# Kernel tuning notes

Measured on AMD Instinct MI355X. Metric: run time of the kernel, lower is better.

## Reference

```python
import jax, jax.numpy as jnp
import numpy as np

T, BATCH, DMODEL, H = 2048, 16, 512, 512


def setup_inputs() -> dict:
    key = jax.random.key(0)
    ks = jax.random.split(key, 8)
    x = jax.random.normal(ks[0], (T, BATCH, DMODEL), jnp.float32)
    # initial carry: (lambda=1, h=0) so the concat trick leaves state untouched
    h0_re = jnp.zeros((1, BATCH, H), jnp.float32)
    h0_im = jnp.zeros((1, BATCH, H), jnp.float32)
    # LRU parameterization (Orvieto et al. 2023): |lambda| in [0.9, 0.99]
    u1 = jax.random.uniform(ks[1], (H,), jnp.float32)
    nu_log = jnp.log(-0.5 * jnp.log(u1 * (0.99 ** 2 - 0.9 ** 2) + 0.9 ** 2))
    theta_log = jnp.log(jax.random.uniform(ks[2], (H,), jnp.float32) * (np.pi / 10) + 1e-4)
    B_re = jax.random.normal(ks[3], (H, DMODEL), jnp.float32) / np.sqrt(2 * DMODEL)
    B_im = jax.random.normal(ks[4], (H, DMODEL), jnp.float32) / np.sqrt(2 * DMODEL)
    C_re = jax.random.normal(ks[5], (DMODEL, H), jnp.float32) / np.sqrt(H)
    C_im = jax.random.normal(ks[6], (DMODEL, H), jnp.float32) / np.sqrt(H)
    D_vec = jax.random.normal(ks[7], (DMODEL,), jnp.float32)
    return dict(x=x, h0_re=h0_re, h0_im=h0_im, nu_log=nu_log, theta_log=theta_log,
                B_re=B_re, B_im=B_im, C_re=C_re, C_im=C_im, D_vec=D_vec)


def _binop(qi, qj):
    # associative combine for h_t = a_t * h_{t-1} + b_t
    a_i, b_i = qi
    a_j, b_j = qj
    return (a_j * a_i, a_j * b_i + b_j)


def reference(x, h0_re, h0_im, nu_log, theta_log, B_re, B_im, C_re, C_im, D_vec):
    # diagonal complex recurrence eigenvalues, |Lambda| = exp(-exp(nu_log)) < 1
    Lam = jnp.exp(-jnp.exp(nu_log) + 1j * jnp.exp(theta_log))        # [H] complex64
    gamma = jnp.sqrt(1.0 - jnp.exp(-2.0 * jnp.exp(nu_log)))           # [H]
    Bmat = (B_re + 1j * B_im) * gamma[:, None]                         # [H, D]
    # map_to_h: Bu elements and broadcast Lambda elements
    Bu = jnp.einsum('tbd,hd->tbh', x.astype(jnp.complex64), Bmat)      # [T, B, H]
    Lam_el = jnp.broadcast_to(Lam, Bu.shape)                            # [T, B, H]
    # concat previous state (lambda=1, b=h0) as first scan element
    h0 = (h0_re + 1j * h0_im).astype(jnp.complex64)                    # [1, B, H]
    a = jnp.concatenate([jnp.ones_like(h0), Lam_el], axis=0)          # [T+1, B, H]
    b = jnp.concatenate([h0, Bu], axis=0)                              # [T+1, B, H]
    _, h_all = jax.lax.associative_scan(_binop, (a, b), axis=0)
    h = h_all[1:]                                                       # [T, B, H]
    # map_from_h: y = Re(C h) + D * x (elementwise skip)
    Cmat = C_re + 1j * C_im                                             # [D, H]
    y = jnp.einsum('tbh,dh->tbd', h, Cmat).real + D_vec * x            # [T, B, D]
    final_state = h[-1:]                                                # [1, B, H]
    return (final_state, y)
```

## Files before the change

### kernel.cpp

```cpp
#include <hip/hip_runtime.h>
#include <stdint.h>

typedef short shortx8 __attribute__((ext_vector_type(8)));
typedef float floatx4 __attribute__((ext_vector_type(4)));

#define T_LEN 2048
#define BATCH 16
#define DMODEL 512
#define HDIM 512
#define M_ROWS (T_LEN * BATCH)
#define NCHUNK 32
#define LCHUNK 64
#define NCHAIN (BATCH * HDIM)
#define Y_ELEMS (M_ROWS * DMODEL)

__device__ __forceinline__ unsigned short f2bf(float f) {
    union { float f; unsigned u; } v; v.f = f;
    unsigned r = (v.u + 0x7FFFu + ((v.u >> 16) & 1u)) >> 16;
    return (unsigned short)r;
}
__device__ __forceinline__ float bf2f(unsigned short u) {
    union { unsigned u; float f; } v; v.u = ((unsigned)u) << 16;
    return v.f;
}

__global__ void prep_kernel(const float* __restrict__ nu_log, const float* __restrict__ th_log,
                            float* lam_re, float* lam_im, float* l64_re, float* l64_im, float* gam) {
    int h = blockIdx.x * blockDim.x + threadIdx.x;
    if (h >= HDIM) return;
    double nu  = exp((double)nu_log[h]);
    double th  = exp((double)th_log[h]);
    double mag = exp(-nu);
    double lre = mag * cos(th), lim = mag * sin(th);
    double g   = sqrt(1.0 - exp(-2.0 * nu));
    double zr = lre, zi = lim;
    for (int i = 0; i < 6; ++i) { double nr = zr*zr - zi*zi; zi = 2.0*zr*zi; zr = nr; }
    lam_re[h] = (float)lre; lam_im[h] = (float)lim;
    l64_re[h] = (float)zr;  l64_im[h] = (float)zi;
    gam[h] = (float)g;
}

__global__ void conv_BC_kernel(const float* __restrict__ B_re, const float* __restrict__ B_im,
                               const float* __restrict__ gam,
                               const float* __restrict__ C_re, const float* __restrict__ C_im,
                               unsigned short* __restrict__ Bs, unsigned short* __restrict__ C2) {
    int idx = blockIdx.x * blockDim.x + threadIdx.x;
    if (idx < 524288) {
        int n = idx >> 9;
        int d = idx & 511;
        int h = n & 511;
        float v = (n < HDIM ? B_re[h * DMODEL + d] : B_im[h * DMODEL + d]) * gam[h];
        Bs[idx] = f2bf(v);
    } else {
        int i2 = idx - 524288;
        int d = i2 >> 10;
        int k = i2 & 1023;
        float v = (k < HDIM) ? C_re[d * HDIM + k] : -C_im[d * HDIM + (k - HDIM)];
        C2[i2] = f2bf(v);
    }
}

__global__ void cast_x_kernel(const float4* __restrict__ x4, unsigned short* __restrict__ xb, int n4) {
    int i = blockIdx.x * blockDim.x + threadIdx.x;
    if (i >= n4) return;
    float4 v = x4[i];
    ushort4 u;
    u.x = f2bf(v.x); u.y = f2bf(v.y); u.z = f2bf(v.z); u.w = f2bf(v.w);
    *(ushort4*)(xb + (size_t)i * 4) = u;
}

template <int MODE>
__global__ __launch_bounds__(256, 4) void gemm_nt(const unsigned short* __restrict__ A,
                                                  const unsigned short* __restrict__ Bmat,
                                                  const int K, const int N, const int lgNB,
                                                  unsigned short* __restrict__ OutB,
                                                  float* __restrict__ OutF,
                                                  const float* __restrict__ Dv,
                                                  const unsigned short* __restrict__ Xb) {
    __shared__ unsigned short As[128 * 64];
    __shared__ unsigned short Bs[128 * 64];
    const int L = blockIdx.x;
    const int xcd = L & 7;
    const int slot = L >> 3;
    const int bn = slot & ((1 << lgNB) - 1);
    const int bm = xcd * 32 + (slot >> lgNB);
    const int tid = threadIdx.x;
    const int wv = tid >> 6, lane = tid & 63;
    const int wr = wv >> 1, wc = wv & 1;
    const int lrow = lane & 15, qq = lane >> 4;
    floatx4 acc[4][4] = {};

    const size_t rowA = (size_t)bm * 128, rowB = (size_t)bn * 128;
    for (int k0 = 0; k0 < K; k0 += 64) {
        #pragma unroll
        for (int j = 0; j < 4; ++j) {
            int ch  = j * 256 + wv * 64 + lane;
            int r   = ch >> 3;
            int c16 = ch & 7;
            int g16 = c16 ^ (r & 7);
            const unsigned short* ga = A    + (rowA + r) * (size_t)K + (k0 + g16 * 8);
            const unsigned short* gb = Bmat + (rowB + r) * (size_t)K + (k0 + g16 * 8);
            unsigned short* la = As + (size_t)(j * 256 + wv * 64) * 8;
            unsigned short* lb = Bs + (size_t)(j * 256 + wv * 64) * 8;
            __builtin_amdgcn_global_load_lds((const __attribute__((address_space(1))) void*)ga,
                                             (__attribute__((address_space(3))) void*)la, 16, 0, 0);
            __builtin_amdgcn_global_load_lds((const __attribute__((address_space(1))) void*)gb,
                                             (__attribute__((address_space(3))) void*)lb, 16, 0, 0);
        }
        __syncthreads();
        #pragma unroll
        for (int s = 0; s < 2; ++s) {
            shortx8 af[4], bf[4];
            #pragma unroll
            for (int mi = 0; mi < 4; ++mi) {
                int row = wr * 64 + mi * 16 + lrow;
                int c16 = (s * 4 + qq) ^ (row & 7);
                af[mi] = *(const shortx8*)&As[row * 64 + c16 * 8];
            }
            #pragma unroll
            for (int ni = 0; ni < 4; ++ni) {
                int row = wc * 64 + ni * 16 + lrow;
                int c16 = (s * 4 + qq) ^ (row & 7);
                bf[ni] = *(const shortx8*)&Bs[row * 64 + c16 * 8];
            }
            #pragma unroll
            for (int mi = 0; mi < 4; ++mi)
                #pragma unroll
                for (int ni = 0; ni < 4; ++ni)
                    acc[mi][ni] = __builtin_amdgcn_mfma_f32_16x16x32_bf16(af[mi], bf[ni], acc[mi][ni], 0, 0, 0);
        }
        __syncthreads();
    }

    #pragma unroll
    for (int mi = 0; mi < 4; ++mi) {
        int mbase = bm * 128 + wr * 64 + mi * 16 + qq * 4;
        #pragma unroll
        for (int ni = 0; ni < 4; ++ni) {
            int n = bn * 128 + wc * 64 + ni * 16 + lrow;
            if (MODE == 0) {
                #pragma unroll
                for (int r = 0; r < 4; ++r)
                    OutB[(size_t)(mbase + r) * N + n] = f2bf(acc[mi][ni][r]);
            } else {
                float dv = Dv[n];
                #pragma unroll
                for (int r = 0; r < 4; ++r) {
                    size_t idx = (size_t)(mbase + r) * N + n;
                    OutF[idx] = acc[mi][ni][r] + dv * bf2f(Xb[idx]);
                }
            }
        }
    }
}

__global__ void scan_partial(const unsigned short* __restrict__ Bu,
                             const float* __restrict__ lam_re, const float* __restrict__ lam_im,
                             float* __restrict__ car_re, float* __restrict__ car_im) {
    int gid = blockIdx.x * blockDim.x + threadIdx.x;
    int chunk = gid >> 12;
    int idx = gid & 4095;
    int b = idx >> 8, hp = idx & 255;
    int h = hp * 2;
    float lr0 = lam_re[h], li0 = lam_im[h];
    float lr1 = lam_re[h + 1], li1 = lam_im[h + 1];
    float v0r = 0.f, v0i = 0.f, v1r = 0.f, v1i = 0.f;
    const unsigned short* p = Bu + (size_t)chunk * LCHUNK * BATCH * 1024 + (size_t)b * 1024 + h;
    for (int j = 0; j < LCHUNK; ++j) {
        unsigned rr = *(const unsigned*)p;
        unsigned ii = *(const unsigned*)(p + 512);
        float b0r = bf2f((unsigned short)rr), b1r = bf2f((unsigned short)(rr >> 16));
        float b0i = bf2f((unsigned short)ii), b1i = bf2f((unsigned short)(ii >> 16));
        float n0r = lr0 * v0r - li0 * v0i + b0r;
        float n0i = lr0 * v0i + li0 * v0r + b0i;
        float n1r = lr1 * v1r - li1 * v1i + b1r;
        float n1i = lr1 * v1i + li1 * v1r + b1i;
        v0r = n0r; v0i = n0i; v1r = n1r; v1i = n1i;
        p += BATCH * 1024;
    }
    int c = b * 512 + h;
    *(float2*)&car_re[chunk * NCHAIN + c] = make_float2(v0r, v1r);
    *(float2*)&car_im[chunk * NCHAIN + c] = make_float2(v0i, v1i);
}

__global__ void scan_apply(unsigned short* __restrict__ Bu,
                           const float* __restrict__ lam_re, const float* __restrict__ lam_im,
                           const float* __restrict__ l64_re, const float* __restrict__ l64_im,
                           const float* __restrict__ h0_re, const float* __restrict__ h0_im,
                           const float* __restrict__ car_re, const float* __restrict__ car_im,
                           float* __restrict__ out_final, int interleave) {
    int gid = blockIdx.x * blockDim.x + threadIdx.x;
    int chunk = gid >> 12;
    int idx = gid & 4095;
    int b = idx >> 8, hp = idx & 255;
    int h = hp * 2;
    int c = b * 512 + h;
    float L0r = l64_re[h], L0i = l64_im[h];
    float L1r = l64_re[h + 1], L1i = l64_im[h + 1];
    float v0r = h0_re[c], v0i = h0_im[c];
    float v1r = h0_re[c + 1], v1i = h0_im[c + 1];
    for (int k = 0; k < chunk; ++k) {
        float2 crr = *(const float2*)&car_re[k * NCHAIN + c];
        float2 cii = *(const float2*)&car_im[k * NCHAIN + c];
        float n0r = L0r * v0r - L0i * v0i + crr.x;
        float n0i = L0r * v0i + L0i * v0r + cii.x;
        float n1r = L1r * v1r - L1i * v1i + crr.y;
        float n1i = L1r * v1i + L1i * v1r + cii.y;
        v0r = n0r; v0i = n0i; v1r = n1r; v1i = n1i;
    }
    float lr0 = lam_re[h], li0 = lam_im[h];
    float lr1 = lam_re[h + 1], li1 = lam_im[h + 1];
    unsigned short* p = Bu + (size_t)chunk * LCHUNK * BATCH * 1024 + (size_t)b * 1024 + h;
    for (int j = 0; j < LCHUNK; ++j) {
        unsigned rr = *(const unsigned*)p;
        unsigned ii = *(const unsigned*)(p + 512);
        float b0r = bf2f((unsigned short)rr), b1r = bf2f((unsigned short)(rr >> 16));
        float b0i = bf2f((unsigned short)ii), b1i = bf2f((unsigned short)(ii >> 16));
        float n0r = lr0 * v0r - li0 * v0i + b0r;
        float n0i = lr0 * v0i + li0 * v0r + b0i;
        float n1r = lr1 * v1r - li1 * v1i + b1r;
        float n1i = lr1 * v1i + li1 * v1r + b1i;
        v0r = n0r; v0i = n0i; v1r = n1r; v1i = n1i;
        *(unsigned*)p         = (unsigned)f2bf(v0r) | ((unsigned)f2bf(v1r) << 16);
        *(unsigned*)(p + 512) = (unsigned)f2bf(v0i) | ((unsigned)f2bf(v1i) << 16);
        p += BATCH * 1024;
    }
    if (chunk == NCHUNK - 1) {
        if (interleave) {
            out_final[2 * c]     = v0r;
            out_final[2 * c + 1] = v0i;
            out_final[2 * c + 2] = v1r;
            out_final[2 * c + 3] = v1i;
        } else {
            out_final[c]     = v0r;
            out_final[c + 1] = v1r;
        }
    }
}

extern "C" void kernel_launch(void* const* d_in, const int* in_sizes, int n_in,
                              void* d_out, int out_size, void* d_ws, size_t ws_size,
                              hipStream_t stream) {
    const float* x        = (const float*)d_in[0];
    const float* h0_re    = (const float*)d_in[1];
    const float* h0_im    = (const float*)d_in[2];
    const float* nu_log   = (const float*)d_in[3];
    const float* theta_lg = (const float*)d_in[4];
    const float* B_re     = (const float*)d_in[5];
    const float* B_im     = (const float*)d_in[6];
    const float* C_re     = (const float*)d_in[7];
    const float* C_im     = (const float*)d_in[8];
    const float* D_vec    = (const float*)d_in[9];

    char* ws = (char*)d_ws;
    unsigned short* BuH  = (unsigned short*)(ws + 0);
    unsigned short* xb   = (unsigned short*)(ws + 67108864);
    unsigned short* Bs   = (unsigned short*)(ws + 100663296);
    unsigned short* C2   = (unsigned short*)(ws + 101711872);
    float* car_re        = (float*)(ws + 102760448);
    float* car_im        = (float*)(ws + 103809024);
    float* lam_re        = (float*)(ws + 104857600);
    float* lam_im        = (float*)(ws + 104859648);
    float* l64_re        = (float*)(ws + 104861696);
    float* l64_im        = (float*)(ws + 104863744);
    float* gam           = (float*)(ws + 104865792);

    int fs_elems = out_size - Y_ELEMS;
    int interleave = (fs_elems == 8192) ? 0 : 1;
    if (fs_elems != 8192) fs_elems = 16384;
    float* out_final = (float*)d_out;
    float* y_out     = (float*)d_out + fs_elems;

    prep_kernel<<<2, 256, 0, stream>>>(nu_log, theta_lg, lam_re, lam_im, l64_re, l64_im, gam);
    conv_BC_kernel<<<(1048576) / 256, 256, 0, stream>>>(B_re, B_im, gam, C_re, C_im, Bs, C2);
    cast_x_kernel<<<(Y_ELEMS / 4) / 256, 256, 0, stream>>>((const float4*)x, xb, Y_ELEMS / 4);
    gemm_nt<0><<<2048, 256, 0, stream>>>(xb, Bs, DMODEL, 1024, 3, BuH, nullptr, nullptr, nullptr);
    scan_partial<<<(NCHUNK * NCHAIN / 2) / 256, 256, 0, stream>>>(BuH, lam_re, lam_im, car_re, car_im);
    scan_apply<<<(NCHUNK * NCHAIN / 2) / 256, 256, 0, stream>>>(BuH, lam_re, lam_im, l64_re, l64_im,
                                                                h0_re, h0_im, car_re, car_im,
                                                                out_final, interleave);
    gemm_nt<1><<<1024, 256, 0, stream>>>(BuH, C2, 1024, 512, 2, nullptr, y_out, D_vec, xb);
}
```

Measured before the change: 256.3 us.

## Replace GEMM with 256x256-tile double-buffered 8-wave pipelined kernel

Both projection GEMMs now use a new kernel with 256x256 output tiles, 512 threads and double-buffered LDS stages. Asynchronous global-to-LDS loads for future k-tiles are interleaved with quarter-tile MFMA phases, using explicit vmcnt/lgkmcnt waits, barriers and setprio. The goal is to hide global-load latency and raise arithmetic intensity per byte loaded. The cost is a much larger LDS footprint and grids of only 512 and 256 blocks, which may underfill the GPU.

Result: slower. 268.0 us (+4.6%).

```diff
diff --git a/kernel.cpp b/kernel.cpp
--- a/kernel.cpp
+++ b/kernel.cpp
@@ -69,85 +69,141 @@
     *(ushort4*)(xb + (size_t)i * 4) = u;
 }
 
+
+#define STAGE_GEN(arr, src, rbase, buf, half, kt) do { \
+    _Pragma("unroll") \
+    for (int j_ = 0; j_ < 2; ++j_) { \
+        int ch_ = j_ * 512 + tid; \
+        int r_ = ch_ >> 3, c_ = ch_ & 7; \
+        int g_ = c_ ^ (r_ & 7); \
+        const unsigned short* gp_ = src + ((rbase) + (size_t)((half) * 128 + r_)) * K + ((kt) * 64 + g_ * 8); \
+        unsigned short* lp_ = &arr[buf][half][0] + ch_ * 8; \
+        __builtin_amdgcn_global_load_lds((const __attribute__((address_space(1))) void*)gp_, \
+            (__attribute__((address_space(3))) void*)lp_, 16, 0, 0); \
+    } } while (0)
+#define STAGE_A(buf, half, kt) STAGE_GEN(As, A,  rowA, buf, half, kt)
+#define STAGE_B(buf, half, kt) STAGE_GEN(Bs, Bm, rowB, buf, half, kt)
+
+#define LDA8(dst, buf, mh) do { \
+    _Pragma("unroll") \
+    for (int mi_ = 0; mi_ < 4; ++mi_) { \
+        int r_ = wr * 64 + mi_ * 16 + lrow; \
+        _Pragma("unroll") \
+        for (int s_ = 0; s_ < 2; ++s_) { \
+            int c_ = (s_ * 4 + qq) ^ (r_ & 7); \
+            dst[mi_][s_] = *(const shortx8*)&As[buf][mh][r_ * 64 + c_ * 8]; \
+        } } } while (0)
+
+#define LDB4(dst, buf, nh) do { \
+    _Pragma("unroll") \
+    for (int ni_ = 0; ni_ < 2; ++ni_) { \
+        int r_ = wc * 32 + ni_ * 16 + lrow; \
+        _Pragma("unroll") \
+        for (int s_ = 0; s_ < 2; ++s_) { \
+            int c_ = (s_ * 4 + qq) ^ (r_ & 7); \
+            dst[ni_][s_] = *(const shortx8*)&Bs[buf][nh][r_ * 64 + c_ * 8]; \
+        } } } while (0)
+
+#define MFMA_Q(mh, nh, AF, BF) do { \
+    _Pragma("unroll") \
+    for (int s_ = 0; s_ < 2; ++s_) \
+    _Pragma("unroll") \
+    for (int mi_ = 0; mi_ < 4; ++mi_) \
+    _Pragma("unroll") \
+    for (int ni_ = 0; ni_ < 2; ++ni_) \
+        acc[mh][mi_][nh][ni_] = __builtin_amdgcn_mfma_f32_16x16x32_bf16(AF[mi_][s_], BF[ni_][s_], acc[mh][mi_][nh][ni_], 0, 0, 0); \
+    } while (0)
+
+#define PHASE_MID do { \
+    __builtin_amdgcn_s_barrier(); \
+    asm volatile("s_waitcnt lgkmcnt(0)" ::: "memory"); \
+    __builtin_amdgcn_s_setprio(1); } while (0)
+
+#define PHASE_END do { \
+    __builtin_amdgcn_s_setprio(0); \
+    asm volatile("s_waitcnt vmcnt(6)" ::: "memory"); \
+    __builtin_amdgcn_s_barrier(); } while (0)
+
 template <int MODE>
-__global__ __launch_bounds__(256, 4) void gemm_nt(const unsigned short* __restrict__ A,
-                                                  const unsigned short* __restrict__ Bmat,
-                                                  const int K, const int N, const int lgNB,
-                                                  unsigned short* __restrict__ OutB,
-                                                  float* __restrict__ OutF,
-                                                  const float* __restrict__ Dv,
-                                                  const unsigned short* __restrict__ Xb) {
-    __shared__ unsigned short As[128 * 64];
-    __shared__ unsigned short Bs[128 * 64];
+__global__ __launch_bounds__(512, 2) void gemm_nt2(const unsigned short* __restrict__ A,
+                                                   const unsigned short* __restrict__ Bm,
+                                                   const int K, const int N, const int lgNB,
+                                                   const int mstride,
+                                                   unsigned short* __restrict__ OutB,
+                                                   float* __restrict__ OutF,
+                                                   const float* __restrict__ Dv,
+                                                   const unsigned short* __restrict__ Xb) {
+    __shared__ __align__(16) unsigned short As[2][2][128 * 64];
+    __shared__ __align__(16) unsigned short Bs[2][2][128 * 64];
     const int L = blockIdx.x;
-    const int xcd = L & 7;
-    const int slot = L >> 3;
+    const int xcd = L & 7, slot = L >> 3;
     const int bn = slot & ((1 << lgNB) - 1);
-    const int bm = xcd * 32 + (slot >> lgNB);
+    const int bm = xcd * mstride + (slot >> lgNB);
     const int tid = threadIdx.x;
-    const int wv = tid >> 6, lane = tid & 63;
-    const int wr = wv >> 1, wc = wv & 1;
+    const int lane = tid & 63, wv = tid >> 6;
+    const int wr = wv >> 2, wc = wv & 3;
     const int lrow = lane & 15, qq = lane >> 4;
-    floatx4 acc[4][4] = {};
-
-    const size_t rowA = (size_t)bm * 128, rowB = (size_t)bn * 128;
-    for (int k0 = 0; k0 < K; k0 += 64) {
-        #pragma unroll
-        for (int j = 0; j < 4; ++j) {
-            int ch  = j * 256 + wv * 64 + lane;
-            int r   = ch >> 3;
-            int c16 = ch & 7;
-            int g16 = c16 ^ (r & 7);
-            const unsigned short* ga = A    + (rowA + r) * (size_t)K + (k0 + g16 * 8);
-            const unsigned short* gb = Bmat + (rowB + r) * (size_t)K + (k0 + g16 * 8);
-            unsigned short* la = As + (size_t)(j * 256 + wv * 64) * 8;
-            unsigned short* lb = Bs + (size_t)(j * 256 + wv * 64) * 8;
-            __builtin_amdgcn_global_load_lds((const __attribute__((address_space(1))) void*)ga,
-                                             (__attribute__((address_space(3))) void*)la, 16, 0, 0);
-            __builtin_amdgcn_global_load_lds((const __attribute__((address_space(1))) void*)gb,
-                                             (__attribute__((address_space(3))) void*)lb, 16, 0, 0);
-        }
-        __syncthreads();
-        #pragma unroll
-        for (int s = 0; s < 2; ++s) {
-            shortx8 af[4], bf[4];
-            #pragma unroll
-            for (int mi = 0; mi < 4; ++mi) {
-                int row = wr * 64 + mi * 16 + lrow;
-                int c16 = (s * 4 + qq) ^ (row & 7);
-                af[mi] = *(const shortx8*)&As[row * 64 + c16 * 8];
-            }
-            #pragma unroll
-            for (int ni = 0; ni < 4; ++ni) {
-                int row = wc * 64 + ni * 16 + lrow;
-                int c16 = (s * 4 + qq) ^ (row & 7);
-                bf[ni] = *(const shortx8*)&Bs[row * 64 + c16 * 8];
-            }
-            #pragma unroll
-            for (int mi = 0; mi < 4; ++mi)
-                #pragma unroll
-                for (int ni = 0; ni < 4; ++ni)
-                    acc[mi][ni] = __builtin_amdgcn_mfma_f32_16x16x32_bf16(af[mi], bf[ni], acc[mi][ni], 0, 0, 0);
-        }
-        __syncthreads();
-    }
-
+    const int NKT = K >> 6, NITER = K >> 7;
+    const size_t rowA = (size_t)bm * 256, rowB = (size_t)bn * 256;
+
+    floatx4 acc[2][4][2][2] = {};
+    shortx8 af[4][2], bf0[2][2], bf1[2][2];
+
+    STAGE_A(0, 0, 0); STAGE_B(0, 0, 0); STAGE_B(0, 1, 0); STAGE_A(0, 1, 0);
+    STAGE_A(1, 0, 1); STAGE_B(1, 0, 1);
+    asm volatile("s_waitcnt vmcnt(8)" ::: "memory");
+    __builtin_amdgcn_s_barrier();
+
+    for (int i = 0; i < NITER; ++i) {
+        int k1 = 2 * i + 1;
+        int k2 = 2 * i + 2; if (k2 > NKT - 1) k2 = NKT - 1;
+        int k3 = 2 * i + 3; if (k3 > NKT - 1) k3 = NKT - 1;
+
+        LDA8(af, 0, 0); LDB4(bf0, 0, 0);
+        STAGE_B(1, 1, k1);
+        PHASE_MID; MFMA_Q(0, 0, af, bf0); PHASE_END;
+        LDB4(bf1, 0, 1);
+        STAGE_A(1, 1, k1);
+        PHASE_MID; MFMA_Q(0, 1, af, bf1); PHASE_END;
+        LDA8(af, 0, 1);
+        STAGE_A(0, 0, k2);
+        PHASE_MID; MFMA_Q(1, 0, af, bf0); PHASE_END;
+        STAGE_B(0, 0, k2);
+        PHASE_MID; MFMA_Q(1, 1, af, bf1); PHASE_END;
+        LDA8(af, 1, 0); LDB4(bf0, 1, 0);
+        STAGE_B(0, 1, k2);
+        PHASE_MID; MFMA_Q(0, 0, af, bf0); PHASE_END;
+        LDB4(bf1, 1, 1);
+        STAGE_A(0, 1, k2);
+        PHASE_MID; MFMA_Q(0, 1, af, bf1); PHASE_END;
+        LDA8(af, 1, 1);
+        STAGE_A(1, 0, k3);
+        PHASE_MID; MFMA_Q(1, 0, af, bf0); PHASE_END;
+        STAGE_B(1, 0, k3);
+        PHASE_MID; MFMA_Q(1, 1, af, bf1); PHASE_END;
+    }
+    asm volatile("s_waitcnt vmcnt(0)" ::: "memory");
+
+    #pragma unroll
+    for (int mh = 0; mh < 2; ++mh)
     #pragma unroll
     for (int mi = 0; mi < 4; ++mi) {
-        int mbase = bm * 128 + wr * 64 + mi * 16 + qq * 4;
+        int mbase = bm * 256 + mh * 128 + wr * 64 + mi * 16 + qq * 4;
         #pragma unroll
-        for (int ni = 0; ni < 4; ++ni) {
-            int n = bn * 128 + wc * 64 + ni * 16 + lrow;
+        for (int nh = 0; nh < 2; ++nh)
+        #pragma unroll
+        for (int ni = 0; ni < 2; ++ni) {
+            int n = bn * 256 + nh * 128 + wc * 32 + ni * 16 + lrow;
             if (MODE == 0) {
                 #pragma unroll
                 for (int r = 0; r < 4; ++r)
-                    OutB[(size_t)(mbase + r) * N + n] = f2bf(acc[mi][ni][r]);
+                    OutB[(size_t)(mbase + r) * N + n] = f2bf(acc[mh][mi][nh][ni][r]);
             } else {
                 float dv = Dv[n];
                 #pragma unroll
                 for (int r = 0; r < 4; ++r) {
                     size_t idx = (size_t)(mbase + r) * N + n;
-                    OutF[idx] = acc[mi][ni][r] + dv * bf2f(Xb[idx]);
+                    OutF[idx] = acc[mh][mi][nh][ni][r] + dv * bf2f(Xb[idx]);
                 }
             }
         }
@@ -274,10 +330,10 @@
     prep_kernel<<<2, 256, 0, stream>>>(nu_log, theta_lg, lam_re, lam_im, l64_re, l64_im, gam);
     conv_BC_kernel<<<(1048576) / 256, 256, 0, stream>>>(B_re, B_im, gam, C_re, C_im, Bs, C2);
     cast_x_kernel<<<(Y_ELEMS / 4) / 256, 256, 0, stream>>>((const float4*)x, xb, Y_ELEMS / 4);
-    gemm_nt<0><<<2048, 256, 0, stream>>>(xb, Bs, DMODEL, 1024, 3, BuH, nullptr, nullptr, nullptr);
+    gemm_nt2<0><<<512, 512, 0, stream>>>(xb, Bs, DMODEL, 1024, 2, 16, BuH, nullptr, nullptr, nullptr);
     scan_partial<<<(NCHUNK * NCHAIN / 2) / 256, 256, 0, stream>>>(BuH, lam_re, lam_im, car_re, car_im);
     scan_apply<<<(NCHUNK * NCHAIN / 2) / 256, 256, 0, stream>>>(BuH, lam_re, lam_im, l64_re, l64_im,
                                                                 h0_re, h0_im, car_re, car_im,
                                                                 out_final, interleave);
-    gemm_nt<1><<<1024, 256, 0, stream>>>(BuH, C2, 1024, 512, 2, nullptr, y_out, D_vec, xb);
-}
+    gemm_nt2<1><<<256, 512, 0, stream>>>(BuH, C2, 1024, 512, 1, 16, nullptr, y_out, D_vec, xb);
+}
```

## Interleave real/imag columns in Bu and scan one complex chain per thread

Applied to the files above, without the earlier changes.

Reorders the B and C weight matrices so real and imaginary parts of each hidden channel sit in adjacent columns. The Bu intermediate therefore holds interleaved complex pairs, and the scan kernels can fetch one 32-bit word per step instead of two loads half a row apart. Each thread now owns a single complex chain, which doubles the thread count and halves per-thread recurrence work, and the carries are stored as float2. The GEMMs are unchanged apart from the permuted weight layout, and the extra threads may lower per-thread instruction-level parallelism.

New measurement: 263.5 us. 1.03x slower.

```diff
diff --git a/kernel.cpp b/kernel.cpp
--- a/kernel.cpp
+++ b/kernel.cpp
@@ -48,14 +48,15 @@
     if (idx < 524288) {
         int n = idx >> 9;
         int d = idx & 511;
-        int h = n & 511;
-        float v = (n < HDIM ? B_re[h * DMODEL + d] : B_im[h * DMODEL + d]) * gam[h];
+        int h = n >> 1;
+        float v = ((n & 1) ? B_im[h * DMODEL + d] : B_re[h * DMODEL + d]) * gam[h];
         Bs[idx] = f2bf(v);
     } else {
         int i2 = idx - 524288;
         int d = i2 >> 10;
         int k = i2 & 1023;
-        float v = (k < HDIM) ? C_re[d * HDIM + k] : -C_im[d * HDIM + (k - HDIM)];
+        int h = k >> 1;
+        float v = (k & 1) ? -C_im[d * HDIM + h] : C_re[d * HDIM + h];
         C2[i2] = f2bf(v);
     }
 }
@@ -156,84 +157,62 @@
 
 __global__ void scan_partial(const unsigned short* __restrict__ Bu,
                              const float* __restrict__ lam_re, const float* __restrict__ lam_im,
-                             float* __restrict__ car_re, float* __restrict__ car_im) {
+                             float2* __restrict__ car) {
     int gid = blockIdx.x * blockDim.x + threadIdx.x;
-    int chunk = gid >> 12;
-    int idx = gid & 4095;
-    int b = idx >> 8, hp = idx & 255;
-    int h = hp * 2;
-    float lr0 = lam_re[h], li0 = lam_im[h];
-    float lr1 = lam_re[h + 1], li1 = lam_im[h + 1];
-    float v0r = 0.f, v0i = 0.f, v1r = 0.f, v1i = 0.f;
-    const unsigned short* p = Bu + (size_t)chunk * LCHUNK * BATCH * 1024 + (size_t)b * 1024 + h;
+    int chunk = gid >> 13;
+    int idx = gid & 8191;
+    int b = idx >> 9, h = idx & 511;
+    float lr = lam_re[h], li = lam_im[h];
+    float vr = 0.f, vi = 0.f;
+    const unsigned short* p = Bu + (size_t)chunk * LCHUNK * BATCH * 1024 + (size_t)b * 1024 + 2 * h;
+    #pragma unroll 4
     for (int j = 0; j < LCHUNK; ++j) {
-        unsigned rr = *(const unsigned*)p;
-        unsigned ii = *(const unsigned*)(p + 512);
-        float b0r = bf2f((unsigned short)rr), b1r = bf2f((unsigned short)(rr >> 16));
-        float b0i = bf2f((unsigned short)ii), b1i = bf2f((unsigned short)(ii >> 16));
-        float n0r = lr0 * v0r - li0 * v0i + b0r;
-        float n0i = lr0 * v0i + li0 * v0r + b0i;
-        float n1r = lr1 * v1r - li1 * v1i + b1r;
-        float n1i = lr1 * v1i + li1 * v1r + b1i;
-        v0r = n0r; v0i = n0i; v1r = n1r; v1i = n1i;
+        unsigned w = *(const unsigned*)p;
+        float br = bf2f((unsigned short)w), bi = bf2f((unsigned short)(w >> 16));
+        float nr = lr * vr - li * vi + br;
+        float ni = lr * vi + li * vr + bi;
+        vr = nr; vi = ni;
         p += BATCH * 1024;
     }
-    int c = b * 512 + h;
-    *(float2*)&car_re[chunk * NCHAIN + c] = make_float2(v0r, v1r);
-    *(float2*)&car_im[chunk * NCHAIN + c] = make_float2(v0i, v1i);
+    car[chunk * NCHAIN + idx] = make_float2(vr, vi);
 }
 
 __global__ void scan_apply(unsigned short* __restrict__ Bu,
                            const float* __restrict__ lam_re, const float* __restrict__ lam_im,
                            const float* __restrict__ l64_re, const float* __restrict__ l64_im,
                            const float* __restrict__ h0_re, const float* __restrict__ h0_im,
-                           const float* __restrict__ car_re, const float* __restrict__ car_im,
+                           const float2* __restrict__ car,
                            float* __restrict__ out_final, int interleave) {
     int gid = blockIdx.x * blockDim.x + threadIdx.x;
-    int chunk = gid >> 12;
-    int idx = gid & 4095;
-    int b = idx >> 8, hp = idx & 255;
-    int h = hp * 2;
-    int c = b * 512 + h;
-    float L0r = l64_re[h], L0i = l64_im[h];
-    float L1r = l64_re[h + 1], L1i = l64_im[h + 1];
-    float v0r = h0_re[c], v0i = h0_im[c];
-    float v1r = h0_re[c + 1], v1i = h0_im[c + 1];
+    int chunk = gid >> 13;
+    int idx = gid & 8191;
+    int b = idx >> 9, h = idx & 511;
+    float Lr = l64_re[h], Li = l64_im[h];
+    float vr = h0_re[idx], vi = h0_im[idx];
     for (int k = 0; k < chunk; ++k) {
-        float2 crr = *(const float2*)&car_re[k * NCHAIN + c];
-        float2 cii = *(const float2*)&car_im[k * NCHAIN + c];
-        float n0r = L0r * v0r - L0i * v0i + crr.x;
-        float n0i = L0r * v0i + L0i * v0r + cii.x;
-        float n1r = L1r * v1r - L1i * v1i + crr.y;
-        float n1i = L1r * v1i + L1i * v1r + cii.y;
-        v0r = n0r; v0i = n0i; v1r = n1r; v1i = n1i;
-    }
-    float lr0 = lam_re[h], li0 = lam_im[h];
-    float lr1 = lam_re[h + 1], li1 = lam_im[h + 1];
-    unsigned short* p = Bu + (size_t)chunk * LCHUNK * BATCH * 1024 + (size_t)b * 1024 + h;
+        float2 cv = car[k * NCHAIN + idx];
+        float nr = Lr * vr - Li * vi + cv.x;
+        float ni = Lr * vi + Li * vr + cv.y;
+        vr = nr; vi = ni;
+    }
+    float lr = lam_re[h], li = lam_im[h];
+    unsigned short* p = Bu + (size_t)chunk * LCHUNK * BATCH * 1024 + (size_t)b * 1024 + 2 * h;
+    #pragma unroll 4
     for (int j = 0; j < LCHUNK; ++j) {
-        unsigned rr = *(const unsigned*)p;
-        unsigned ii = *(const unsigned*)(p + 512);
-        float b0r = bf2f((unsigned short)rr), b1r = bf2f((unsigned short)(rr >> 16));
-        float b0i = bf2f((unsigned short)ii), b1i = bf2f((unsigned short)(ii >> 16));
-        float n0r = lr0 * v0r - li0 * v0i + b0r;
-        float n0i = lr0 * v0i + li0 * v0r + b0i;
-        float n1r = lr1 * v1r - li1 * v1i + b1r;
-        float n1i = lr1 * v1i + li1 * v1r + b1i;
-        v0r = n0r; v0i = n0i; v1r = n1r; v1i = n1i;
-        *(unsigned*)p         = (unsigned)f2bf(v0r) | ((unsigned)f2bf(v1r) << 16);
-        *(unsigned*)(p + 512) = (unsigned)f2bf(v0i) | ((unsigned)f2bf(v1i) << 16);
+        unsigned w = *(const unsigned*)p;
+        float br = bf2f((unsigned short)w), bi = bf2f((unsigned short)(w >> 16));
+        float nr = lr * vr - li * vi + br;
+        float ni = lr * vi + li * vr + bi;
+        vr = nr; vi = ni;
+        *(unsigned*)p = (unsigned)f2bf(vr) | ((unsigned)f2bf(vi) << 16);
         p += BATCH * 1024;
     }
     if (chunk == NCHUNK - 1) {
         if (interleave) {
-            out_final[2 * c]     = v0r;
-            out_final[2 * c + 1] = v0i;
-            out_final[2 * c + 2] = v1r;
-            out_final[2 * c + 3] = v1i;
+            out_final[2 * idx]     = vr;
+            out_final[2 * idx + 1] = vi;
         } else {
-            out_final[c]     = v0r;
-            out_final[c + 1] = v1r;
+            out_final[idx] = vr;
         }
     }
 }
@@ -257,8 +236,7 @@
     unsigned short* xb   = (unsigned short*)(ws + 67108864);
     unsigned short* Bs   = (unsigned short*)(ws + 100663296);
     unsigned short* C2   = (unsigned short*)(ws + 101711872);
-    float* car_re        = (float*)(ws + 102760448);
-    float* car_im        = (float*)(ws + 103809024);
+    float2* car          = (float2*)(ws + 102760448);
     float* lam_re        = (float*)(ws + 104857600);
     float* lam_im        = (float*)(ws + 104859648);
     float* l64_re        = (float*)(ws + 104861696);
@@ -275,9 +253,9 @@
     conv_BC_kernel<<<(1048576) / 256, 256, 0, stream>>>(B_re, B_im, gam, C_re, C_im, Bs, C2);
     cast_x_kernel<<<(Y_ELEMS / 4) / 256, 256, 0, stream>>>((const float4*)x, xb, Y_ELEMS / 4);
     gemm_nt<0><<<2048, 256, 0, stream>>>(xb, Bs, DMODEL, 1024, 3, BuH, nullptr, nullptr, nullptr);
-    scan_partial<<<(NCHUNK * NCHAIN / 2) / 256, 256, 0, stream>>>(BuH, lam_re, lam_im, car_re, car_im);
-    scan_apply<<<(NCHUNK * NCHAIN / 2) / 256, 256, 0, stream>>>(BuH, lam_re, lam_im, l64_re, l64_im,
-                                                                h0_re, h0_im, car_re, car_im,
-                                                                out_final, interleave);
+    scan_partial<<<(NCHUNK * NCHAIN) / 256, 256, 0, stream>>>(BuH, lam_re, lam_im, car);
+    scan_apply<<<(NCHUNK * NCHAIN) / 256, 256, 0, stream>>>(BuH, lam_re, lam_im, l64_re, l64_im,
+                                                            h0_re, h0_im, car,
+                                                            out_final, interleave);
     gemm_nt<1><<<1024, 256, 0, stream>>>(BuH, C2, 1024, 512, 2, nullptr, y_out, D_vec, xb);
 }
```
